# Optimization experiments

Hardware: AMD Instinct MI355X
Metric: run time of the kernel (lower is better)

## Reference

```python
import jax, jax.numpy as jnp
import numpy as np

B, S, U = 64, 64, 16
EMB = 10
D = U - 2 + 2 * EMB      # encoder d_model = 34
DD = 3                   # decoder d_model
FF = 4                   # dim_feedforward
NL = 4                   # num layers (enc and dec)
ENH = 2                  # encoder heads
WV, SV = 10000, 400      # word / syllable vocab sizes


def _ln(x, w, b, eps=1e-5):
    mu = jnp.mean(x, -1, keepdims=True)
    var = jnp.mean((x - mu) ** 2, -1, keepdims=True)
    return (x - mu) / jnp.sqrt(var + eps) * w + b


def _mha(xq, xkv, qkv_w, qkv_b, out_w, out_b, nhead, mask=None):
    d = xq.shape[-1]
    wq, wk, wv = jnp.split(qkv_w, 3, axis=0)
    bq, bk, bv = jnp.split(qkv_b, 3, axis=0)
    q = xq @ wq.T + bq
    k = xkv @ wk.T + bk
    v = xkv @ wv.T + bv
    b_, sq, sk = q.shape[0], q.shape[1], k.shape[1]
    dh = d // nhead
    q = q.reshape(b_, sq, nhead, dh)
    k = k.reshape(b_, sk, nhead, dh)
    v = v.reshape(b_, sk, nhead, dh)
    scores = jnp.einsum('bqhd,bkhd->bhqk', q, k) * (1.0 / np.sqrt(dh))
    if mask is not None:
        scores = scores + mask
    attn = jax.nn.softmax(scores, axis=-1)
    out = jnp.einsum('bhqk,bkhd->bqhd', attn, v).reshape(b_, sq, d)
    return out @ out_w.T + out_b


def _pos_encoding(batch, d_model):
    # Faithful to the original quirk: pe has shape [max_len, 1, d] and is added
    # to a batch-first [B,S,D] tensor as x + pe[:B]  ->  row b of pe is added
    # to ALL sequence positions of batch element b.
    pos = jnp.arange(batch, dtype=jnp.float32)[:, None]
    div = jnp.exp(jnp.arange(0, d_model, 2, dtype=jnp.float32) * (-np.log(10000.0) / d_model))
    ang = pos * div  # [B, D/2]
    pe = jnp.stack([jnp.sin(ang), jnp.cos(ang)], axis=-1).reshape(batch, d_model)
    return pe[:, None, :]  # [B,1,D]


def setup_inputs() -> dict:
    key = jax.random.key(0)
    ks = iter(jax.random.split(key, 64))

    def n(shape, s=0.1):
        return jax.random.normal(next(ks), shape, dtype=jnp.float32) * s

    base = jax.random.uniform(next(ks), (B, S, U), dtype=jnp.float32)
    widx = jax.random.randint(next(ks), (B, S), 0, WV).astype(jnp.float32)
    sidx = jax.random.randint(next(ks), (B, S), 0, SV).astype(jnp.float32)
    src = base.at[:, :, U - 2].set(widx).at[:, :, U - 1].set(sidx)
    return {
        'src': src,
        'word_emb': jax.random.uniform(next(ks), (WV, EMB), jnp.float32, -0.1, 0.1),
        'syll_emb': jax.random.uniform(next(ks), (SV, EMB), jnp.float32, -0.1, 0.1),
        'enc_qkv_w': n((NL, 3 * D, D)), 'enc_qkv_b': jnp.zeros((NL, 3 * D)),
        'enc_out_w': n((NL, D, D)), 'enc_out_b': jnp.zeros((NL, D)),
        'enc_ln1_w': jnp.ones((NL, D)), 'enc_ln1_b': jnp.zeros((NL, D)),
        'enc_lin1_w': n((NL, FF, D)), 'enc_lin1_b': jnp.zeros((NL, FF)),
        'enc_lin2_w': n((NL, D, FF)), 'enc_lin2_b': jnp.zeros((NL, D)),
        'enc_ln2_w': jnp.ones((NL, D)), 'enc_ln2_b': jnp.zeros((NL, D)),
        'norm_w': jnp.ones((D,)), 'norm_b': jnp.zeros((D,)),
        'eo_w': jax.random.uniform(next(ks), (DD, D), jnp.float32, -0.1, 0.1),
        'eo_b': jnp.zeros((DD,)),
        'dec_sa_qkv_w': n((NL, 3 * DD, DD)), 'dec_sa_qkv_b': jnp.zeros((NL, 3 * DD)),
        'dec_sa_out_w': n((NL, DD, DD)), 'dec_sa_out_b': jnp.zeros((NL, DD)),
        'dec_ln1_w': jnp.ones((NL, DD)), 'dec_ln1_b': jnp.zeros((NL, DD)),
        'dec_ca_qkv_w': n((NL, 3 * DD, DD)), 'dec_ca_qkv_b': jnp.zeros((NL, 3 * DD)),
        'dec_ca_out_w': n((NL, DD, DD)), 'dec_ca_out_b': jnp.zeros((NL, DD)),
        'dec_ln2_w': jnp.ones((NL, DD)), 'dec_ln2_b': jnp.zeros((NL, DD)),
        'dec_lin1_w': n((NL, FF, DD)), 'dec_lin1_b': jnp.zeros((NL, FF)),
        'dec_lin2_w': n((NL, DD, FF)), 'dec_lin2_b': jnp.zeros((NL, DD)),
        'dec_ln3_w': jnp.ones((NL, DD)), 'dec_ln3_b': jnp.zeros((NL, DD)),
    }


def reference(src, word_emb, syll_emb,
              enc_qkv_w, enc_qkv_b, enc_out_w, enc_out_b,
              enc_ln1_w, enc_ln1_b, enc_lin1_w, enc_lin1_b,
              enc_lin2_w, enc_lin2_b, enc_ln2_w, enc_ln2_b,
              norm_w, norm_b, eo_w, eo_b,
              dec_sa_qkv_w, dec_sa_qkv_b, dec_sa_out_w, dec_sa_out_b,
              dec_ln1_w, dec_ln1_b,
              dec_ca_qkv_w, dec_ca_qkv_b, dec_ca_out_w, dec_ca_out_b,
              dec_ln2_w, dec_ln2_b,
              dec_lin1_w, dec_lin1_b, dec_lin2_w, dec_lin2_b,
              dec_ln3_w, dec_ln3_b):
    b, s = src.shape[0], src.shape[1]
    # embed_lyrics
    widx = src[:, :, U - 2].astype(jnp.int32)
    sidx = src[:, :, U - 1].astype(jnp.int32)
    x = jnp.concatenate([src[:, :, :U - 2], word_emb[widx], syll_emb[sidx]], axis=2)  # [B,S,D]
    x = x + _pos_encoding(b, D)
    # TransformerEncoder (post-norm, relu, dropout=0) + final LayerNorm
    for l in range(NL):
        sa = _mha(x, x, enc_qkv_w[l], enc_qkv_b[l], enc_out_w[l], enc_out_b[l], ENH)
        x = _ln(x + sa, enc_ln1_w[l], enc_ln1_b[l])
        ff = jax.nn.relu(x @ enc_lin1_w[l].T + enc_lin1_b[l]) @ enc_lin2_w[l].T + enc_lin2_b[l]
        x = _ln(x + ff, enc_ln2_w[l], enc_ln2_b[l])
    x = _ln(x, norm_w, norm_b)
    memory = x @ eo_w.T + eo_b  # [B,S,3]

    causal = jnp.where(jnp.tril(jnp.ones((s, s), bool)), 0.0, -1e9).astype(jnp.float32)

    def decode(tgt):
        y = tgt
        for l in range(NL):
            sa = _mha(y, y, dec_sa_qkv_w[l], dec_sa_qkv_b[l], dec_sa_out_w[l], dec_sa_out_b[l], 1, causal)
            y = _ln(y + sa, dec_ln1_w[l], dec_ln1_b[l])
            ca = _mha(y, memory, dec_ca_qkv_w[l], dec_ca_qkv_b[l], dec_ca_out_w[l], dec_ca_out_b[l], 1)
            y = _ln(y + ca, dec_ln2_w[l], dec_ln2_b[l])
            ff = jax.nn.relu(y @ dec_lin1_w[l].T + dec_lin1_b[l]) @ dec_lin2_w[l].T + dec_lin2_b[l]
            y = _ln(y + ff, dec_ln3_w[l], dec_ln3_b[l])
        return y

    # mask, position i only depends on tgt[:, :i+1], so a fixed-size padded
    # buffer + scan computes identical values.
    def step(tgt, i):
        out_i = jax.lax.dynamic_slice_in_dim(decode(tgt), i, 1, axis=1)  # [B,1,3]
        return jax.lax.dynamic_update_slice(tgt, out_i, (0, i + 1, 0)), None

    tgt0 = jnp.zeros((b, s, DD), jnp.float32)
    tgt, _ = jax.lax.scan(step, tgt0, jnp.arange(s - 1))
    return jnp.concatenate([tgt, src[:, :, U - 2:U - 1], src[:, :, U - 1:U]], axis=2)
```

## Files before the change

kernel.cpp:

```cpp
#include <hip/hip_runtime.h>
#include <math.h>

#define B_ 64
#define S_ 64
#define U_ 16
#define EMB_ 10
#define D_ 34
#define DD_ 3
#define FF_ 4
#define NL_ 4

__global__ __launch_bounds__(512) void enc_kernel(
    const float* __restrict__ src, const float* __restrict__ wemb,
    const float* __restrict__ semb,
    const float* __restrict__ qkv_w, const float* __restrict__ qkv_b,
    const float* __restrict__ out_w, const float* __restrict__ out_b,
    const float* __restrict__ ln1_w, const float* __restrict__ ln1_b,
    const float* __restrict__ lin1_w, const float* __restrict__ lin1_b,
    const float* __restrict__ lin2_w, const float* __restrict__ lin2_b,
    const float* __restrict__ ln2_w, const float* __restrict__ ln2_b,
    const float* __restrict__ norm_w, const float* __restrict__ norm_b,
    const float* __restrict__ eo_w, const float* __restrict__ eo_b,
    float* __restrict__ mem, float* __restrict__ out)
{
    const int b = blockIdx.x;
    const int tid = threadIdx.x;

    __shared__ float xs[S_][D_ + 1];
    __shared__ float qs[S_][D_];
    __shared__ float ks[S_][D_];
    __shared__ float vs[S_][D_];
    __shared__ float att[S_][D_];
    __shared__ float ffh[S_][FF_];
    __shared__ float tmp[S_][D_ + 1];
    __shared__ float pacc[4][128][19];
    __shared__ float wq_s[3 * D_ * D_];
    __shared__ float wo_s[D_ * D_];
    __shared__ float w1_s[FF_ * D_];
    __shared__ float w2_s[D_ * FF_];
    __shared__ float bq_s[3 * D_], bo_s[D_], b1_s[FF_], b2_s[D_];
    __shared__ float l1w_s[D_], l1b_s[D_], l2w_s[D_], l2b_s[D_];

    const float negln = -logf(10000.0f) / (float)D_;
    #pragma unroll
    for (int rep = 0; rep < 5; ++rep) {
        int idx = tid + rep * 512;
        if (idx < S_ * D_) {
            int pos = idx / D_, d = idx % D_;
            float v;
            if (d < U_ - 2) {
                v = src[(b * S_ + pos) * U_ + d];
            } else if (d < U_ - 2 + EMB_) {
                int wi = (int)src[(b * S_ + pos) * U_ + (U_ - 2)];
                v = wemb[wi * EMB_ + (d - (U_ - 2))];
            } else {
                int si = (int)src[(b * S_ + pos) * U_ + (U_ - 1)];
                v = semb[si * EMB_ + (d - (U_ - 2 + EMB_))];
            }
            int k = d >> 1;
            float div = expf((float)(2 * k) * negln);
            float ang = (float)b * div;
            v += (d & 1) ? cosf(ang) : sinf(ang);
            xs[pos][d] = v;
        }
    }
    __syncthreads();

    const float rs17 = 0.24253562503633297f;

    for (int l = 0; l < NL_; ++l) {
        for (int t = tid; t < 3 * D_ * D_; t += 512) wq_s[t] = qkv_w[l * 3 * D_ * D_ + t];
        for (int t = tid; t < D_ * D_; t += 512)     wo_s[t] = out_w[l * D_ * D_ + t];
        for (int t = tid; t < FF_ * D_; t += 512)    w1_s[t] = lin1_w[l * FF_ * D_ + t];
        for (int t = tid; t < D_ * FF_; t += 512)    w2_s[t] = lin2_w[l * D_ * FF_ + t];
        for (int t = tid; t < 3 * D_ + 6 * D_ + FF_; t += 512) {
            if      (t < 3 * D_)          bq_s[t]            = qkv_b[l * 3 * D_ + t];
            else if (t < 3 * D_ + D_)     bo_s[t - 3 * D_]   = out_b[l * D_ + (t - 3 * D_)];
            else if (t < 3 * D_ + 2 * D_) l1w_s[t - 4 * D_]  = ln1_w[l * D_ + (t - 4 * D_)];
            else if (t < 3 * D_ + 3 * D_) l1b_s[t - 5 * D_]  = ln1_b[l * D_ + (t - 5 * D_)];
            else if (t < 3 * D_ + 4 * D_) l2w_s[t - 6 * D_]  = ln2_w[l * D_ + (t - 6 * D_)];
            else if (t < 3 * D_ + 5 * D_) l2b_s[t - 7 * D_]  = ln2_b[l * D_ + (t - 7 * D_)];
            else if (t < 3 * D_ + 6 * D_) b2_s[t - 8 * D_]   = lin2_b[l * D_ + (t - 8 * D_)];
            else                          b1_s[t - 9 * D_]   = lin1_b[l * FF_ + (t - 9 * D_)];
        }
        __syncthreads();

        #pragma unroll 2
        for (int rep = 0; rep < 13; ++rep) {
            int idx = tid + rep * 512;
            if (idx < S_ * 3 * D_) {
                int pos = idx / (3 * D_), r = idx % (3 * D_);
                const float* wrow = wq_s + r * D_;
                float aE = bq_s[r], aO = 0.f;
                #pragma unroll
                for (int d = 0; d < D_; d += 2) {
                    aE += xs[pos][d] * wrow[d];
                    aO += xs[pos][d + 1] * wrow[d + 1];
                }
                float acc = aE + aO;
                if (r < D_)          qs[pos][r] = acc;
                else if (r < 2 * D_) ks[pos][r - D_] = acc;
                else                 vs[pos][r - 2 * D_] = acc;
            }
        }
        __syncthreads();

        {
            int c = tid >> 7, hq = tid & 127;
            int h = hq >> 6, qi = hq & 63;
            int off = h * 17;
            float qv[17], acc[17];
            #pragma unroll
            for (int d = 0; d < 17; ++d) { qv[d] = qs[qi][off + d]; acc[d] = 0.f; }
            float ssum = 0.f;
            int j0 = c * 16;
            #pragma unroll 2
            for (int jj = 0; jj < 16; ++jj) {
                int j = j0 + jj;
                float sE = 0.f, sO = 0.f;
                #pragma unroll
                for (int d = 0; d < 16; d += 2) {
                    sE += qv[d] * ks[j][off + d];
                    sO += qv[d + 1] * ks[j][off + d + 1];
                }
                float sc = sE + sO + qv[16] * ks[j][off + 16];
                float e = __expf(sc * rs17);
                ssum += e;
                #pragma unroll
                for (int d = 0; d < 17; ++d) acc[d] += e * vs[j][off + d];
            }
            #pragma unroll
            for (int d = 0; d < 17; ++d) pacc[c][hq][d] = acc[d];
            pacc[c][hq][17] = ssum;
        }
        __syncthreads();

        if (tid < 128) {
            int h = tid >> 6, qi = tid & 63;
            int off = h * 17;
            float ssum = pacc[0][tid][17] + pacc[1][tid][17] +
                         pacc[2][tid][17] + pacc[3][tid][17];
            float inv = 1.f / ssum;
            #pragma unroll
            for (int d = 0; d < 17; ++d)
                att[qi][off + d] = (pacc[0][tid][d] + pacc[1][tid][d] +
                                    pacc[2][tid][d] + pacc[3][tid][d]) * inv;
        }
        __syncthreads();

        #pragma unroll 2
        for (int rep = 0; rep < 5; ++rep) {
            int idx = tid + rep * 512;
            if (idx < S_ * D_) {
                int pos = idx / D_, d = idx % D_;
                const float* wrow = wo_s + d * D_;
                float aE = bo_s[d], aO = 0.f;
                #pragma unroll
                for (int e = 0; e < D_; e += 2) {
                    aE += att[pos][e] * wrow[e];
                    aO += att[pos][e + 1] * wrow[e + 1];
                }
                tmp[pos][d] = xs[pos][d] + aE + aO;
            }
        }
        __syncthreads();

        if (tid < S_) {
            int row = tid;
            float sA = 0.f, sB = 0.f;
            #pragma unroll
            for (int d = 0; d < D_; d += 2) { sA += tmp[row][d]; sB += tmp[row][d + 1]; }
            float mu = (sA + sB) * (1.0f / D_);
            float vA = 0.f, vB = 0.f;
            #pragma unroll
            for (int d = 0; d < D_; d += 2) {
                float t0 = tmp[row][d] - mu;     vA += t0 * t0;
                float t1 = tmp[row][d + 1] - mu; vB += t1 * t1;
            }
            float rstd = rsqrtf((vA + vB) * (1.0f / D_) + 1e-5f);
            #pragma unroll
            for (int d = 0; d < D_; ++d)
                xs[row][d] = (tmp[row][d] - mu) * rstd * l1w_s[d] + l1b_s[d];
        }
        __syncthreads();

        if (tid < 256) {
            int pos = tid >> 2, f = tid & 3;
            const float* wrow = w1_s + f * D_;
            float aE = b1_s[f], aO = 0.f;
            #pragma unroll
            for (int d = 0; d < D_; d += 2) {
                aE += xs[pos][d] * wrow[d];
                aO += xs[pos][d + 1] * wrow[d + 1];
            }
            ffh[pos][f] = fmaxf(aE + aO, 0.f);
        }
        __syncthreads();

        #pragma unroll 2
        for (int rep = 0; rep < 5; ++rep) {
            int idx = tid + rep * 512;
            if (idx < S_ * D_) {
                int pos = idx / D_, d = idx % D_;
                const float* wrow = w2_s + d * FF_;
                float acc = b2_s[d] + ffh[pos][0] * wrow[0] + ffh[pos][1] * wrow[1] +
                            ffh[pos][2] * wrow[2] + ffh[pos][3] * wrow[3];
                tmp[pos][d] = xs[pos][d] + acc;
            }
        }
        __syncthreads();

        if (tid < S_) {
            int row = tid;
            float sA = 0.f, sB = 0.f;
            #pragma unroll
            for (int d = 0; d < D_; d += 2) { sA += tmp[row][d]; sB += tmp[row][d + 1]; }
            float mu = (sA + sB) * (1.0f / D_);
            float vA = 0.f, vB = 0.f;
            #pragma unroll
            for (int d = 0; d < D_; d += 2) {
                float t0 = tmp[row][d] - mu;     vA += t0 * t0;
                float t1 = tmp[row][d + 1] - mu; vB += t1 * t1;
            }
            float rstd = rsqrtf((vA + vB) * (1.0f / D_) + 1e-5f);
            #pragma unroll
            for (int d = 0; d < D_; ++d)
                xs[row][d] = (tmp[row][d] - mu) * rstd * l2w_s[d] + l2b_s[d];
        }
        __syncthreads();
    }

    if (tid < S_) {
        int row = tid;
        float sA = 0.f, sB = 0.f;
        #pragma unroll
        for (int d = 0; d < D_; d += 2) { sA += xs[row][d]; sB += xs[row][d + 1]; }
        float mu = (sA + sB) * (1.0f / D_);
        float vA = 0.f, vB = 0.f;
        #pragma unroll
        for (int d = 0; d < D_; d += 2) {
            float t0 = xs[row][d] - mu;     vA += t0 * t0;
            float t1 = xs[row][d + 1] - mu; vB += t1 * t1;
        }
        float rstd = rsqrtf((vA + vB) * (1.0f / D_) + 1e-5f);
        #pragma unroll
        for (int d = 0; d < D_; ++d)
            xs[row][d] = (xs[row][d] - mu) * rstd * norm_w[d] + norm_b[d];
    }
    __syncthreads();

    if (tid < S_ * DD_) {
        int pos = tid / DD_, r = tid % DD_;
        const float* wrow = eo_w + r * D_;
        float aE = eo_b[r], aO = 0.f;
        #pragma unroll
        for (int d = 0; d < D_; d += 2) {
            aE += xs[pos][d] * wrow[d];
            aO += xs[pos][d + 1] * wrow[d + 1];
        }
        mem[(b * S_ + pos) * DD_ + r] = aE + aO;
    }

    if (tid < S_) {
        out[(b * S_ + tid) * 5 + 3] = src[(b * S_ + tid) * U_ + (U_ - 2)];
        out[(b * S_ + tid) * 5 + 4] = src[(b * S_ + tid) * U_ + (U_ - 1)];
    }
}

#define PIN(x) asm volatile("" : "+v"(x))

template <int CTRL>
__device__ __forceinline__ float dpp_add(float v) {
    int t = __builtin_amdgcn_update_dpp(0, __float_as_int(v), CTRL, 0xf, 0xf, true);
    return v + __int_as_float(t);
}

__device__ __forceinline__ float wave_sum_l63(float v) {
    v = dpp_add<0x111>(v);
    v = dpp_add<0x112>(v);
    v = dpp_add<0x114>(v);
    v = dpp_add<0x118>(v);
    v = dpp_add<0x142>(v);
    v = dpp_add<0x143>(v);
    return v;
}

__device__ __forceinline__ float bcast63(float v) {
    return __int_as_float(__builtin_amdgcn_readlane(__float_as_int(v), 63));
}

__device__ __forceinline__ void ln3n(float z0, float z1, float z2,
                                     float w0, float w1, float w2,
                                     float b0, float b1, float b2,
                                     float& o0, float& o1, float& o2) {
    float mu = (z0 + z1 + z2) * (1.0f / 3.0f);
    float d0 = z0 - mu, d1 = z1 - mu, d2 = z2 - mu;
    float var = (d0 * d0 + d1 * d1 + d2 * d2) * (1.0f / 3.0f);
    float rstd = __builtin_amdgcn_rsqf(var + 1e-5f);
    o0 = d0 * rstd * w0 + b0;
    o1 = d1 * rstd * w1 + b1;
    o2 = d2 * rstd * w2 + b2;
}

__global__ __launch_bounds__(64, 1) void dec_kernel(
    const float* __restrict__ mem,
    const float* __restrict__ sa_qkv_w, const float* __restrict__ sa_qkv_b,
    const float* __restrict__ sa_out_w, const float* __restrict__ sa_out_b,
    const float* __restrict__ gln1_w, const float* __restrict__ gln1_b,
    const float* __restrict__ ca_qkv_w, const float* __restrict__ ca_qkv_b,
    const float* __restrict__ ca_out_w, const float* __restrict__ ca_out_b,
    const float* __restrict__ gln2_w, const float* __restrict__ gln2_b,
    const float* __restrict__ l1_w, const float* __restrict__ l1_b,
    const float* __restrict__ l2_w, const float* __restrict__ l2_b,
    const float* __restrict__ gln3_w, const float* __restrict__ gln3_b,
    float* __restrict__ out)
{
    const int b = blockIdx.x;
    const int lane = threadIdx.x;
    const float rs3 = 0.5773502691896258f;

    __shared__ __align__(16) float fst[NL_][40];
    for (int t = lane; t < NL_ * 40; t += 64) {
        int l = t / 40, s = t % 40;
        float v = 0.f;
        if      (s < 12) v = l1_w[l * 12 + s];
        else if (s < 16) v = l1_b[l * 4 + (s - 12)];
        else if (s < 28) v = l2_w[l * 12 + (s - 16)];
        else if (s < 31) v = l2_b[l * 3 + (s - 28)];
        else if (s < 34) v = gln3_w[l * 3 + (s - 31)];
        else if (s < 37) v = gln3_b[l * 3 + (s - 34)];
        fst[l][s] = v;
    }
    __syncthreads();

    float Wsq[NL_][9][3], Bsq[NL_][9];
    float Wso[NL_][3][3], Bso[NL_][3];
    float N1w[NL_][3], N1b[NL_][3];
    float Wcq[NL_][3][3], Bcq[NL_][3];
    float Wco[NL_][3][3], Bco[NL_][3];
    float N2w[NL_][3], N2b[NL_][3];

    #pragma unroll
    for (int l = 0; l < NL_; ++l) {
        #pragma unroll
        for (int r = 0; r < 9; ++r) {
            float sc = (r < 3) ? rs3 : 1.0f;
            Bsq[l][r] = sa_qkv_b[l * 9 + r] * sc;
            #pragma unroll
            for (int c = 0; c < 3; ++c) Wsq[l][r][c] = sa_qkv_w[l * 27 + r * 3 + c] * sc;
        }
        #pragma unroll
        for (int r = 0; r < 3; ++r) {
            Bso[l][r] = sa_out_b[l * 3 + r];
            Bcq[l][r] = ca_qkv_b[l * 9 + r] * rs3;
            Bco[l][r] = ca_out_b[l * 3 + r];
            N1w[l][r] = gln1_w[l * 3 + r];  N1b[l][r] = gln1_b[l * 3 + r];
            N2w[l][r] = gln2_w[l * 3 + r];  N2b[l][r] = gln2_b[l * 3 + r];
            #pragma unroll
            for (int c = 0; c < 3; ++c) {
                Wso[l][r][c] = sa_out_w[l * 9 + r * 3 + c];
                Wcq[l][r][c] = ca_qkv_w[l * 27 + r * 3 + c] * rs3;
                Wco[l][r][c] = ca_out_w[l * 9 + r * 3 + c];
            }
        }
    }

    float m0 = mem[(b * S_ + lane) * DD_ + 0];
    float m1 = mem[(b * S_ + lane) * DD_ + 1];
    float m2 = mem[(b * S_ + lane) * DD_ + 2];

    float ck[NL_][3], cv[NL_][3];
    #pragma unroll
    for (int l = 0; l < NL_; ++l) {
        #pragma unroll
        for (int r = 0; r < 3; ++r) {
            ck[l][r] = ca_qkv_w[l * 27 + (3 + r) * 3 + 0] * m0 +
                       ca_qkv_w[l * 27 + (3 + r) * 3 + 1] * m1 +
                       ca_qkv_w[l * 27 + (3 + r) * 3 + 2] * m2 + ca_qkv_b[l * 9 + 3 + r];
            cv[l][r] = ca_qkv_w[l * 27 + (6 + r) * 3 + 0] * m0 +
                       ca_qkv_w[l * 27 + (6 + r) * 3 + 1] * m1 +
                       ca_qkv_w[l * 27 + (6 + r) * 3 + 2] * m2 + ca_qkv_b[l * 9 + 6 + r];
        }
    }

    #pragma unroll
    for (int l = 0; l < NL_; ++l) {
        #pragma unroll
        for (int r = 0; r < 9; ++r) {
            PIN(Bsq[l][r]);
            #pragma unroll
            for (int c = 0; c < 3; ++c) PIN(Wsq[l][r][c]);
        }
        #pragma unroll
        for (int r = 0; r < 3; ++r) {
            PIN(Bso[l][r]); PIN(Bcq[l][r]); PIN(Bco[l][r]);
            PIN(N1w[l][r]); PIN(N1b[l][r]); PIN(N2w[l][r]); PIN(N2b[l][r]);
            #pragma unroll
            for (int c = 0; c < 3; ++c) { PIN(Wso[l][r][c]); PIN(Wcq[l][r][c]); PIN(Wco[l][r][c]); }
        }
    }

    float sk[NL_][3] = {{0.f}}, sv[NL_][3] = {{0.f}};

    if (lane < 3) out[(b * S_ + 0) * 5 + lane] = 0.f;

    float y0 = 0.f, y1 = 0.f, y2 = 0.f;

    for (int i = 0; i < S_ - 1; ++i) {
        #pragma unroll
        for (int l = 0; l < NL_; ++l) {
            float wv[40];
            {
                const float4* fp = (const float4*)fst[l];
                #pragma unroll
                for (int k = 0; k < 10; ++k) {
                    float4 t4 = fp[k];
                    wv[4 * k + 0] = t4.x; wv[4 * k + 1] = t4.y;
                    wv[4 * k + 2] = t4.z; wv[4 * k + 3] = t4.w;
                }
                #pragma unroll
                for (int k = 0; k < 37; ++k) PIN(wv[k]);
            }

            float q[3], kn[3], vn[3];
            #pragma unroll
            for (int r = 0; r < 3; ++r) {
                q[r]  = Wsq[l][r][0] * y0 + Wsq[l][r][1] * y1 + Wsq[l][r][2] * y2 + Bsq[l][r];
                kn[r] = Wsq[l][3 + r][0] * y0 + Wsq[l][3 + r][1] * y1 + Wsq[l][3 + r][2] * y2 + Bsq[l][3 + r];
                vn[r] = Wsq[l][6 + r][0] * y0 + Wsq[l][6 + r][1] * y1 + Wsq[l][6 + r][2] * y2 + Bsq[l][6 + r];
            }
            if (lane == i) {
                #pragma unroll
                for (int r = 0; r < 3; ++r) { sk[l][r] = kn[r]; sv[l][r] = vn[r]; }
            }
            float sc = q[0] * sk[l][0] + q[1] * sk[l][1] + q[2] * sk[l][2];
            float e = (lane <= i) ? __expf(sc) : 0.f;
            float es  = wave_sum_l63(e);
            float ev0 = wave_sum_l63(e * sv[l][0]);
            float ev1 = wave_sum_l63(e * sv[l][1]);
            float ev2 = wave_sum_l63(e * sv[l][2]);
            float inv = __builtin_amdgcn_rcpf(bcast63(es));
            float a0 = bcast63(ev0) * inv, a1 = bcast63(ev1) * inv, a2 = bcast63(ev2) * inv;
            float s0 = Wso[l][0][0] * a0 + Wso[l][0][1] * a1 + Wso[l][0][2] * a2 + Bso[l][0];
            float s1 = Wso[l][1][0] * a0 + Wso[l][1][1] * a1 + Wso[l][1][2] * a2 + Bso[l][1];
            float s2 = Wso[l][2][0] * a0 + Wso[l][2][1] * a1 + Wso[l][2][2] * a2 + Bso[l][2];
            ln3n(y0 + s0, y1 + s1, y2 + s2,
                 N1w[l][0], N1w[l][1], N1w[l][2], N1b[l][0], N1b[l][1], N1b[l][2],
                 y0, y1, y2);

            float p0 = Wcq[l][0][0] * y0 + Wcq[l][0][1] * y1 + Wcq[l][0][2] * y2 + Bcq[l][0];
            float p1 = Wcq[l][1][0] * y0 + Wcq[l][1][1] * y1 + Wcq[l][1][2] * y2 + Bcq[l][1];
            float p2 = Wcq[l][2][0] * y0 + Wcq[l][2][1] * y1 + Wcq[l][2][2] * y2 + Bcq[l][2];
            float sc2 = p0 * ck[l][0] + p1 * ck[l][1] + p2 * ck[l][2];
            float e2 = __expf(sc2);
            float cs  = wave_sum_l63(e2);
            float cw0 = wave_sum_l63(e2 * cv[l][0]);
            float cw1 = wave_sum_l63(e2 * cv[l][1]);
            float cw2 = wave_sum_l63(e2 * cv[l][2]);
            inv = __builtin_amdgcn_rcpf(bcast63(cs));
            a0 = bcast63(cw0) * inv; a1 = bcast63(cw1) * inv; a2 = bcast63(cw2) * inv;
            float c0 = Wco[l][0][0] * a0 + Wco[l][0][1] * a1 + Wco[l][0][2] * a2 + Bco[l][0];
            float c1 = Wco[l][1][0] * a0 + Wco[l][1][1] * a1 + Wco[l][1][2] * a2 + Bco[l][1];
            float c2 = Wco[l][2][0] * a0 + Wco[l][2][1] * a1 + Wco[l][2][2] * a2 + Bco[l][2];
            ln3n(y0 + c0, y1 + c1, y2 + c2,
                 N2w[l][0], N2w[l][1], N2w[l][2], N2b[l][0], N2b[l][1], N2b[l][2],
                 y0, y1, y2);

            float h[4];
            #pragma unroll
            for (int f = 0; f < 4; ++f)
                h[f] = fmaxf(wv[f * 3 + 0] * y0 + wv[f * 3 + 1] * y1 + wv[f * 3 + 2] * y2 + wv[12 + f], 0.f);
            float f0 = wv[16] * h[0] + wv[17] * h[1] + wv[18] * h[2] + wv[19] * h[3] + wv[28];
            float f1 = wv[20] * h[0] + wv[21] * h[1] + wv[22] * h[2] + wv[23] * h[3] + wv[29];
            float f2 = wv[24] * h[0] + wv[25] * h[1] + wv[26] * h[2] + wv[27] * h[3] + wv[30];
            ln3n(y0 + f0, y1 + f1, y2 + f2,
                 wv[31], wv[32], wv[33], wv[34], wv[35], wv[36],
                 y0, y1, y2);
        }
        if (lane == 0) {
            out[(b * S_ + i + 1) * 5 + 0] = y0;
            out[(b * S_ + i + 1) * 5 + 1] = y1;
            out[(b * S_ + i + 1) * 5 + 2] = y2;
        }
    }
}

extern "C" void kernel_launch(void* const* d_in, const int* in_sizes, int n_in,
                              void* d_out, int out_size, void* d_ws, size_t ws_size,
                              hipStream_t stream) {
    const float* src  = (const float*)d_in[0];
    const float* wemb = (const float*)d_in[1];
    const float* semb = (const float*)d_in[2];

    float* mem = (float*)d_ws;
    float* out = (float*)d_out;

    enc_kernel<<<B_, 512, 0, stream>>>(
        src, wemb, semb,
        (const float*)d_in[3],  (const float*)d_in[4],
        (const float*)d_in[5],  (const float*)d_in[6],
        (const float*)d_in[7],  (const float*)d_in[8],
        (const float*)d_in[9],  (const float*)d_in[10],
        (const float*)d_in[11], (const float*)d_in[12],
        (const float*)d_in[13], (const float*)d_in[14],
        (const float*)d_in[15], (const float*)d_in[16],
        (const float*)d_in[17], (const float*)d_in[18],
        mem, out);

    dec_kernel<<<B_, 64, 0, stream>>>(
        mem,
        (const float*)d_in[19], (const float*)d_in[20],
        (const float*)d_in[21], (const float*)d_in[22],
        (const float*)d_in[23], (const float*)d_in[24],
        (const float*)d_in[25], (const float*)d_in[26],
        (const float*)d_in[27], (const float*)d_in[28],
        (const float*)d_in[29], (const float*)d_in[30],
        (const float*)d_in[31], (const float*)d_in[32],
        (const float*)d_in[33], (const float*)d_in[34],
        (const float*)d_in[35], (const float*)d_in[36],
        out);
}
```

Measured before the change: 377.8 us.

## Fold attention output projections into value weights and exploit LayerNorm scale invariance

Precomposes the self-attention value projection with the output projection, and the cross-attention value with its output projection, so each attention result already lives in model space. It then skips the softmax normalisation by scaling the residual by the exp-sum and relying on LayerNorm's scale invariance. It also switches to exp2 with log2e folded into the query weights, masks with an additive bias instead of a select, and moves the FFN weights from shared memory into pinned registers. The aim is to shorten the serial per-step dependency chain (no reciprocal, no output matvec, no LDS reads). The trade-offs are a single-pass variance formula with slightly different numerics, more register pressure, and the eps term no longer matching exactly once the values are scaled.

Result: slower. 398.5 us (+5.5%).

```diff
diff --git a/kernel.cpp b/kernel.cpp
--- a/kernel.cpp
+++ b/kernel.cpp
@@ -289,17 +289,18 @@
     return __int_as_float(__builtin_amdgcn_readlane(__float_as_int(v), 63));
 }
 
-__device__ __forceinline__ void ln3n(float z0, float z1, float z2,
+__device__ __forceinline__ void ln3e(float z0, float z1, float z2,
                                      float w0, float w1, float w2,
                                      float b0, float b1, float b2,
                                      float& o0, float& o1, float& o2) {
-    float mu = (z0 + z1 + z2) * (1.0f / 3.0f);
-    float d0 = z0 - mu, d1 = z1 - mu, d2 = z2 - mu;
-    float var = (d0 * d0 + d1 * d1 + d2 * d2) * (1.0f / 3.0f);
-    float rstd = __builtin_amdgcn_rsqf(var + 1e-5f);
-    o0 = d0 * rstd * w0 + b0;
-    o1 = d1 * rstd * w1 + b1;
-    o2 = d2 * rstd * w2 + b2;
+    float s1 = (z0 + z1) + z2;
+    float s2 = fmaf(z0, z0, fmaf(z1, z1, z2 * z2));
+    float mu = s1 * (1.0f / 3.0f);
+    float vpe = fmaf(s2, (1.0f / 3.0f), fmaf(-mu, mu, 1e-5f));
+    float rstd = __builtin_amdgcn_rsqf(vpe);
+    o0 = fmaf(z0 - mu, rstd * w0, b0);
+    o1 = fmaf(z1 - mu, rstd * w1, b1);
+    o2 = fmaf(z2 - mu, rstd * w2, b2);
 }
 
 __global__ __launch_bounds__(64, 1) void dec_kernel(
@@ -317,51 +318,61 @@
 {
     const int b = blockIdx.x;
     const int lane = threadIdx.x;
+    const float LOG2E = 1.4426950408889634f;
     const float rs3 = 0.5773502691896258f;
-
-    __shared__ __align__(16) float fst[NL_][40];
-    for (int t = lane; t < NL_ * 40; t += 64) {
-        int l = t / 40, s = t % 40;
-        float v = 0.f;
-        if      (s < 12) v = l1_w[l * 12 + s];
-        else if (s < 16) v = l1_b[l * 4 + (s - 12)];
-        else if (s < 28) v = l2_w[l * 12 + (s - 16)];
-        else if (s < 31) v = l2_b[l * 3 + (s - 28)];
-        else if (s < 34) v = gln3_w[l * 3 + (s - 31)];
-        else if (s < 37) v = gln3_b[l * 3 + (s - 34)];
-        fst[l][s] = v;
-    }
-    __syncthreads();
-
-    float Wsq[NL_][9][3], Bsq[NL_][9];
-    float Wso[NL_][3][3], Bso[NL_][3];
+    const float QS = rs3 * LOG2E;
+
+    float Wqp[NL_][3][3], Bqp[NL_][3];
+    float Wk [NL_][3][3], Bk [NL_][3];
+    float WVp[NL_][3][3], bvp[NL_][3];
+    float Bso[NL_][3];
+    float Wcq[NL_][3][3], Bcq[NL_][3];
+    float Bco[NL_][3];
     float N1w[NL_][3], N1b[NL_][3];
-    float Wcq[NL_][3][3], Bcq[NL_][3];
-    float Wco[NL_][3][3], Bco[NL_][3];
     float N2w[NL_][3], N2b[NL_][3];
+    float F1w[NL_][4][3], F1b[NL_][4];
+    float F2w[NL_][3][4], F2b[NL_][3];
+    float N3w[NL_][3], N3b[NL_][3];
 
     #pragma unroll
     for (int l = 0; l < NL_; ++l) {
         #pragma unroll
-        for (int r = 0; r < 9; ++r) {
-            float sc = (r < 3) ? rs3 : 1.0f;
-            Bsq[l][r] = sa_qkv_b[l * 9 + r] * sc;
-            #pragma unroll
-            for (int c = 0; c < 3; ++c) Wsq[l][r][c] = sa_qkv_w[l * 27 + r * 3 + c] * sc;
-        }
-        #pragma unroll
         for (int r = 0; r < 3; ++r) {
+            Bqp[l][r] = sa_qkv_b[l * 9 + r] * QS;
+            Bk [l][r] = sa_qkv_b[l * 9 + 3 + r];
+            #pragma unroll
+            for (int c = 0; c < 3; ++c) {
+                Wqp[l][r][c] = sa_qkv_w[l * 27 + r * 3 + c] * QS;
+                Wk [l][r][c] = sa_qkv_w[l * 27 + (3 + r) * 3 + c];
+            }
+            float a0 = 0.f, a1 = 0.f, a2 = 0.f, ab = 0.f;
+            #pragma unroll
+            for (int t = 0; t < 3; ++t) {
+                float wso = sa_out_w[l * 9 + r * 3 + t];
+                a0 += wso * sa_qkv_w[l * 27 + (6 + t) * 3 + 0];
+                a1 += wso * sa_qkv_w[l * 27 + (6 + t) * 3 + 1];
+                a2 += wso * sa_qkv_w[l * 27 + (6 + t) * 3 + 2];
+                ab += wso * sa_qkv_b[l * 9 + 6 + t];
+            }
+            WVp[l][r][0] = a0; WVp[l][r][1] = a1; WVp[l][r][2] = a2;
+            bvp[l][r] = ab;
             Bso[l][r] = sa_out_b[l * 3 + r];
-            Bcq[l][r] = ca_qkv_b[l * 9 + r] * rs3;
+            Bcq[l][r] = ca_qkv_b[l * 9 + r];
             Bco[l][r] = ca_out_b[l * 3 + r];
+            #pragma unroll
+            for (int c = 0; c < 3; ++c) Wcq[l][r][c] = ca_qkv_w[l * 27 + r * 3 + c];
             N1w[l][r] = gln1_w[l * 3 + r];  N1b[l][r] = gln1_b[l * 3 + r];
             N2w[l][r] = gln2_w[l * 3 + r];  N2b[l][r] = gln2_b[l * 3 + r];
-            #pragma unroll
-            for (int c = 0; c < 3; ++c) {
-                Wso[l][r][c] = sa_out_w[l * 9 + r * 3 + c];
-                Wcq[l][r][c] = ca_qkv_w[l * 27 + r * 3 + c] * rs3;
-                Wco[l][r][c] = ca_out_w[l * 9 + r * 3 + c];
-            }
+            N3w[l][r] = gln3_w[l * 3 + r];  N3b[l][r] = gln3_b[l * 3 + r];
+            F2b[l][r] = l2_b[l * 3 + r];
+            #pragma unroll
+            for (int c = 0; c < 4; ++c) F2w[l][r][c] = l2_w[l * 12 + r * 4 + c];
+        }
+        #pragma unroll
+        for (int f = 0; f < 4; ++f) {
+            F1b[l][f] = l1_b[l * 4 + f];
+            #pragma unroll
+            for (int c = 0; c < 3; ++c) F1w[l][f][c] = l1_w[l * 12 + f * 3 + c];
         }
     }
 
@@ -369,34 +380,49 @@
     float m1 = mem[(b * S_ + lane) * DD_ + 1];
     float m2 = mem[(b * S_ + lane) * DD_ + 2];
 
-    float ck[NL_][3], cv[NL_][3];
+    float ck[NL_][3], cvp[NL_][3];
     #pragma unroll
     for (int l = 0; l < NL_; ++l) {
+        float cvt[3];
+        #pragma unroll
+        for (int t = 0; t < 3; ++t) {
+            cvt[t] = ca_qkv_w[l * 27 + (6 + t) * 3 + 0] * m0 +
+                     ca_qkv_w[l * 27 + (6 + t) * 3 + 1] * m1 +
+                     ca_qkv_w[l * 27 + (6 + t) * 3 + 2] * m2 + ca_qkv_b[l * 9 + 6 + t];
+        }
         #pragma unroll
         for (int r = 0; r < 3; ++r) {
-            ck[l][r] = ca_qkv_w[l * 27 + (3 + r) * 3 + 0] * m0 +
+            float kk = ca_qkv_w[l * 27 + (3 + r) * 3 + 0] * m0 +
                        ca_qkv_w[l * 27 + (3 + r) * 3 + 1] * m1 +
                        ca_qkv_w[l * 27 + (3 + r) * 3 + 2] * m2 + ca_qkv_b[l * 9 + 3 + r];
-            cv[l][r] = ca_qkv_w[l * 27 + (6 + r) * 3 + 0] * m0 +
-                       ca_qkv_w[l * 27 + (6 + r) * 3 + 1] * m1 +
-                       ca_qkv_w[l * 27 + (6 + r) * 3 + 2] * m2 + ca_qkv_b[l * 9 + 6 + r];
+            ck[l][r] = kk * QS;
+            cvp[l][r] = ca_out_w[l * 9 + r * 3 + 0] * cvt[0] +
+                        ca_out_w[l * 9 + r * 3 + 1] * cvt[1] +
+                        ca_out_w[l * 9 + r * 3 + 2] * cvt[2];
         }
     }
 
     #pragma unroll
     for (int l = 0; l < NL_; ++l) {
         #pragma unroll
-        for (int r = 0; r < 9; ++r) {
-            PIN(Bsq[l][r]);
-            #pragma unroll
-            for (int c = 0; c < 3; ++c) PIN(Wsq[l][r][c]);
-        }
-        #pragma unroll
         for (int r = 0; r < 3; ++r) {
-            PIN(Bso[l][r]); PIN(Bcq[l][r]); PIN(Bco[l][r]);
+            PIN(Bqp[l][r]); PIN(Bk[l][r]); PIN(bvp[l][r]); PIN(Bso[l][r]);
+            PIN(Bcq[l][r]); PIN(Bco[l][r]);
             PIN(N1w[l][r]); PIN(N1b[l][r]); PIN(N2w[l][r]); PIN(N2b[l][r]);
-            #pragma unroll
-            for (int c = 0; c < 3; ++c) { PIN(Wso[l][r][c]); PIN(Wcq[l][r][c]); PIN(Wco[l][r][c]); }
+            PIN(N3w[l][r]); PIN(N3b[l][r]); PIN(F2b[l][r]);
+            PIN(ck[l][r]); PIN(cvp[l][r]);
+            #pragma unroll
+            for (int c = 0; c < 3; ++c) {
+                PIN(Wqp[l][r][c]); PIN(Wk[l][r][c]); PIN(WVp[l][r][c]); PIN(Wcq[l][r][c]);
+            }
+            #pragma unroll
+            for (int c = 0; c < 4; ++c) PIN(F2w[l][r][c]);
+        }
+        #pragma unroll
+        for (int f = 0; f < 4; ++f) {
+            PIN(F1b[l][f]);
+            #pragma unroll
+            for (int c = 0; c < 3; ++c) PIN(F1w[l][f][c]);
         }
     }
 
@@ -407,75 +433,60 @@
     float y0 = 0.f, y1 = 0.f, y2 = 0.f;
 
     for (int i = 0; i < S_ - 1; ++i) {
+        float msa = (lane <= i) ? 0.f : -1.0e30f;
         #pragma unroll
         for (int l = 0; l < NL_; ++l) {
-            float wv[40];
-            {
-                const float4* fp = (const float4*)fst[l];
-                #pragma unroll
-                for (int k = 0; k < 10; ++k) {
-                    float4 t4 = fp[k];
-                    wv[4 * k + 0] = t4.x; wv[4 * k + 1] = t4.y;
-                    wv[4 * k + 2] = t4.z; wv[4 * k + 3] = t4.w;
-                }
-                #pragma unroll
-                for (int k = 0; k < 37; ++k) PIN(wv[k]);
-            }
-
-            float q[3], kn[3], vn[3];
-            #pragma unroll
-            for (int r = 0; r < 3; ++r) {
-                q[r]  = Wsq[l][r][0] * y0 + Wsq[l][r][1] * y1 + Wsq[l][r][2] * y2 + Bsq[l][r];
-                kn[r] = Wsq[l][3 + r][0] * y0 + Wsq[l][3 + r][1] * y1 + Wsq[l][3 + r][2] * y2 + Bsq[l][3 + r];
-                vn[r] = Wsq[l][6 + r][0] * y0 + Wsq[l][6 + r][1] * y1 + Wsq[l][6 + r][2] * y2 + Bsq[l][6 + r];
-            }
+            float q0 = fmaf(Wqp[l][0][0], y0, fmaf(Wqp[l][0][1], y1, fmaf(Wqp[l][0][2], y2, Bqp[l][0])));
+            float q1 = fmaf(Wqp[l][1][0], y0, fmaf(Wqp[l][1][1], y1, fmaf(Wqp[l][1][2], y2, Bqp[l][1])));
+            float q2 = fmaf(Wqp[l][2][0], y0, fmaf(Wqp[l][2][1], y1, fmaf(Wqp[l][2][2], y2, Bqp[l][2])));
+            float k0 = fmaf(Wk[l][0][0], y0, fmaf(Wk[l][0][1], y1, fmaf(Wk[l][0][2], y2, Bk[l][0])));
+            float k1 = fmaf(Wk[l][1][0], y0, fmaf(Wk[l][1][1], y1, fmaf(Wk[l][1][2], y2, Bk[l][1])));
+            float k2 = fmaf(Wk[l][2][0], y0, fmaf(Wk[l][2][1], y1, fmaf(Wk[l][2][2], y2, Bk[l][2])));
+            float v0 = fmaf(WVp[l][0][0], y0, fmaf(WVp[l][0][1], y1, fmaf(WVp[l][0][2], y2, bvp[l][0])));
+            float v1 = fmaf(WVp[l][1][0], y0, fmaf(WVp[l][1][1], y1, fmaf(WVp[l][1][2], y2, bvp[l][1])));
+            float v2 = fmaf(WVp[l][2][0], y0, fmaf(WVp[l][2][1], y1, fmaf(WVp[l][2][2], y2, bvp[l][2])));
             if (lane == i) {
-                #pragma unroll
-                for (int r = 0; r < 3; ++r) { sk[l][r] = kn[r]; sv[l][r] = vn[r]; }
-            }
-            float sc = q[0] * sk[l][0] + q[1] * sk[l][1] + q[2] * sk[l][2];
-            float e = (lane <= i) ? __expf(sc) : 0.f;
-            float es  = wave_sum_l63(e);
-            float ev0 = wave_sum_l63(e * sv[l][0]);
-            float ev1 = wave_sum_l63(e * sv[l][1]);
-            float ev2 = wave_sum_l63(e * sv[l][2]);
-            float inv = __builtin_amdgcn_rcpf(bcast63(es));
-            float a0 = bcast63(ev0) * inv, a1 = bcast63(ev1) * inv, a2 = bcast63(ev2) * inv;
-            float s0 = Wso[l][0][0] * a0 + Wso[l][0][1] * a1 + Wso[l][0][2] * a2 + Bso[l][0];
-            float s1 = Wso[l][1][0] * a0 + Wso[l][1][1] * a1 + Wso[l][1][2] * a2 + Bso[l][1];
-            float s2 = Wso[l][2][0] * a0 + Wso[l][2][1] * a1 + Wso[l][2][2] * a2 + Bso[l][2];
-            ln3n(y0 + s0, y1 + s1, y2 + s2,
-                 N1w[l][0], N1w[l][1], N1w[l][2], N1b[l][0], N1b[l][1], N1b[l][2],
-                 y0, y1, y2);
-
-            float p0 = Wcq[l][0][0] * y0 + Wcq[l][0][1] * y1 + Wcq[l][0][2] * y2 + Bcq[l][0];
-            float p1 = Wcq[l][1][0] * y0 + Wcq[l][1][1] * y1 + Wcq[l][1][2] * y2 + Bcq[l][1];
-            float p2 = Wcq[l][2][0] * y0 + Wcq[l][2][1] * y1 + Wcq[l][2][2] * y2 + Bcq[l][2];
-            float sc2 = p0 * ck[l][0] + p1 * ck[l][1] + p2 * ck[l][2];
-            float e2 = __expf(sc2);
-            float cs  = wave_sum_l63(e2);
-            float cw0 = wave_sum_l63(e2 * cv[l][0]);
-            float cw1 = wave_sum_l63(e2 * cv[l][1]);
-            float cw2 = wave_sum_l63(e2 * cv[l][2]);
-            inv = __builtin_amdgcn_rcpf(bcast63(cs));
-            a0 = bcast63(cw0) * inv; a1 = bcast63(cw1) * inv; a2 = bcast63(cw2) * inv;
-            float c0 = Wco[l][0][0] * a0 + Wco[l][0][1] * a1 + Wco[l][0][2] * a2 + Bco[l][0];
-            float c1 = Wco[l][1][0] * a0 + Wco[l][1][1] * a1 + Wco[l][1][2] * a2 + Bco[l][1];
-            float c2 = Wco[l][2][0] * a0 + Wco[l][2][1] * a1 + Wco[l][2][2] * a2 + Bco[l][2];
-            ln3n(y0 + c0, y1 + c1, y2 + c2,
-                 N2w[l][0], N2w[l][1], N2w[l][2], N2b[l][0], N2b[l][1], N2b[l][2],
-                 y0, y1, y2);
-
-            float h[4];
-            #pragma unroll
-            for (int f = 0; f < 4; ++f)
-                h[f] = fmaxf(wv[f * 3 + 0] * y0 + wv[f * 3 + 1] * y1 + wv[f * 3 + 2] * y2 + wv[12 + f], 0.f);
-            float f0 = wv[16] * h[0] + wv[17] * h[1] + wv[18] * h[2] + wv[19] * h[3] + wv[28];
-            float f1 = wv[20] * h[0] + wv[21] * h[1] + wv[22] * h[2] + wv[23] * h[3] + wv[29];
-            float f2 = wv[24] * h[0] + wv[25] * h[1] + wv[26] * h[2] + wv[27] * h[3] + wv[30];
-            ln3n(y0 + f0, y1 + f1, y2 + f2,
-                 wv[31], wv[32], wv[33], wv[34], wv[35], wv[36],
-                 y0, y1, y2);
+                sk[l][0] = k0; sk[l][1] = k1; sk[l][2] = k2;
+                sv[l][0] = v0; sv[l][1] = v1; sv[l][2] = v2;
+            }
+            float sc = fmaf(q0, sk[l][0], fmaf(q1, sk[l][1], fmaf(q2, sk[l][2], msa)));
+            float e = __builtin_amdgcn_exp2f(sc);
+            float es  = bcast63(wave_sum_l63(e));
+            float ev0 = bcast63(wave_sum_l63(e * sv[l][0]));
+            float ev1 = bcast63(wave_sum_l63(e * sv[l][1]));
+            float ev2 = bcast63(wave_sum_l63(e * sv[l][2]));
+            float t0 = y0 + Bso[l][0], t1 = y1 + Bso[l][1], t2 = y2 + Bso[l][2];
+            float z0 = fmaf(t0, es, ev0);
+            float z1 = fmaf(t1, es, ev1);
+            float z2 = fmaf(t2, es, ev2);
+            ln3e(z0, z1, z2, N1w[l][0], N1w[l][1], N1w[l][2],
+                 N1b[l][0], N1b[l][1], N1b[l][2], y0, y1, y2);
+
+            float p0 = fmaf(Wcq[l][0][0], y0, fmaf(Wcq[l][0][1], y1, fmaf(Wcq[l][0][2], y2, Bcq[l][0])));
+            float p1 = fmaf(Wcq[l][1][0], y0, fmaf(Wcq[l][1][1], y1, fmaf(Wcq[l][1][2], y2, Bcq[l][1])));
+            float p2 = fmaf(Wcq[l][2][0], y0, fmaf(Wcq[l][2][1], y1, fmaf(Wcq[l][2][2], y2, Bcq[l][2])));
+            float sc2 = fmaf(p0, ck[l][0], fmaf(p1, ck[l][1], p2 * ck[l][2]));
+            float e2 = __builtin_amdgcn_exp2f(sc2);
+            float cs  = bcast63(wave_sum_l63(e2));
+            float cw0 = bcast63(wave_sum_l63(e2 * cvp[l][0]));
+            float cw1 = bcast63(wave_sum_l63(e2 * cvp[l][1]));
+            float cw2 = bcast63(wave_sum_l63(e2 * cvp[l][2]));
+            float u0 = y0 + Bco[l][0], u1 = y1 + Bco[l][1], u2 = y2 + Bco[l][2];
+            z0 = fmaf(u0, cs, cw0);
+            z1 = fmaf(u1, cs, cw1);
+            z2 = fmaf(u2, cs, cw2);
+            ln3e(z0, z1, z2, N2w[l][0], N2w[l][1], N2w[l][2],
+                 N2b[l][0], N2b[l][1], N2b[l][2], y0, y1, y2);
+
+            float h0 = fmaxf(fmaf(F1w[l][0][0], y0, fmaf(F1w[l][0][1], y1, fmaf(F1w[l][0][2], y2, F1b[l][0]))), 0.f);
+            float h1 = fmaxf(fmaf(F1w[l][1][0], y0, fmaf(F1w[l][1][1], y1, fmaf(F1w[l][1][2], y2, F1b[l][1]))), 0.f);
+            float h2 = fmaxf(fmaf(F1w[l][2][0], y0, fmaf(F1w[l][2][1], y1, fmaf(F1w[l][2][2], y2, F1b[l][2]))), 0.f);
+            float h3 = fmaxf(fmaf(F1w[l][3][0], y0, fmaf(F1w[l][3][1], y1, fmaf(F1w[l][3][2], y2, F1b[l][3]))), 0.f);
+            float f0 = fmaf(F2w[l][0][0], h0, fmaf(F2w[l][0][1], h1, fmaf(F2w[l][0][2], h2, fmaf(F2w[l][0][3], h3, F2b[l][0]))));
+            float f1 = fmaf(F2w[l][1][0], h0, fmaf(F2w[l][1][1], h1, fmaf(F2w[l][1][2], h2, fmaf(F2w[l][1][3], h3, F2b[l][1]))));
+            float f2 = fmaf(F2w[l][2][0], h0, fmaf(F2w[l][2][1], h1, fmaf(F2w[l][2][2], h2, fmaf(F2w[l][2][3], h3, F2b[l][2]))));
+            ln3e(y0 + f0, y1 + f1, y2 + f2, N3w[l][0], N3w[l][1], N3w[l][2],
+                 N3b[l][0], N3b[l][1], N3b[l][2], y0, y1, y2);
         }
         if (lane == 0) {
             out[(b * S_ + i + 1) * 5 + 0] = y0;
```
